# Optimization experiments

Hardware: AMD Instinct MI355X
Metric: run time of the kernel (lower is better)

The kernel has to match this reference:

```python
import jax, jax.numpy as jnp
import numpy as np

PATCH_NUM = 10  # self.patch_num divisor
TOP_N = 5


def _extract_patches(feat, ps):
    """feat: [1,C,H,W] -> [P, C*ps*ps] with P = (H-ps)*(W-ps), matching the
    original loop over h in range(H-ps), w in range(W-ps)."""
    C, H, W = feat.shape[1:]
    Hm, Wm = H - ps, W - ps
    shifts = [feat[0, :, i:i + Hm, j:j + Wm] for i in range(ps) for j in range(ps)]
    patches = jnp.stack(shifts, axis=1)          # [C, ps*ps, Hm, Wm]
    return patches.reshape(C * ps * ps, Hm * Wm).T  # [P, K], P index = h*Wm + w


def _scale_loss(src_f, tgt_f, pos, ps):
    C = src_f.shape[1]
    K = C * ps * ps
    patches = _extract_patches(src_f, ps)  # [P, K]

    def per_target(p):
        th, tw = p[0], p[1]
        tpatch = jax.lax.dynamic_slice(tgt_f, (0, 0, th, tw), (1, C, ps, ps)).reshape(K)
        dist = jnp.sum(jnp.abs(patches - tpatch), axis=1)  # [P] summed L1 per patch
        _, ids = jax.lax.top_k(-dist, TOP_N)                # 5 nearest patches
        sel = patches[ids]                                   # [TOP_N, K]
        # sum over top-n of mean-L1, each divided by top_n (as in original)
        return jnp.sum(jnp.mean(jnp.abs(sel - tpatch), axis=1)) / TOP_N

    # sequential map over the small number of target patches keeps peak memory
    # at one [P,K] abs-diff buffer per step
    return jnp.sum(jax.lax.map(per_target, pos))


def setup_inputs() -> dict:
    key = jax.random.key(0)
    k0, k1, k2, k3, k4, k5 = jax.random.split(key, 6)
    return {
        "src_f0": jax.random.normal(k0, (1, 64, 256, 256), dtype=jnp.float32),
        "tgt_f0": jax.random.normal(k1, (1, 64, 256, 256), dtype=jnp.float32),
        "src_f1": jax.random.normal(k2, (1, 128, 128, 128), dtype=jnp.float32),
        "tgt_f1": jax.random.normal(k3, (1, 128, 128, 128), dtype=jnp.float32),
        "pos0": jax.random.randint(k4, (10, 2), 0, 253, dtype=jnp.int32),
        "pos1": jax.random.randint(k5, (5, 2), 0, 127, dtype=jnp.int32),
    }


def reference(src_f0, tgt_f0, src_f1, tgt_f1, pos0, pos1):
    loss = _scale_loss(src_f0, tgt_f0, pos0, 3) + _scale_loss(src_f1, tgt_f1, pos1, 1)
    return loss / PATCH_NUM
```

## Files before the change

### kernel.cpp

```cpp
#include <hip/hip_runtime.h>
#include <hip/hip_bf16.h>

#define BIG 3.4e38f


__device__ __forceinline__ void merge5(float a[5], const float* b) {
    float r[5];
#pragma unroll
    for (int k = 0; k < 5; ++k) {
        float best = BIG;
#pragma unroll
        for (int i = 0; i <= k + 1; ++i) {
            const int j = k + 1 - i;
            float va = (i == 0) ? -BIG : a[i - 1];
            float vb = (j == 0) ? -BIG : b[j - 1];
            best = fminf(best, fmaxf(va, vb));
        }
        r[k] = best;
    }
#pragma unroll
    for (int k = 0; k < 5; ++k) a[k] = r[k];
}

__device__ __forceinline__ void top5_insert(float m[5], float d) {
    if (d < m[4]) {
        m[4] = d;
#pragma unroll
        for (int k = 4; k > 0; --k) {
            float lo = fminf(m[k - 1], m[k]);
            float hi = fmaxf(m[k - 1], m[k]);
            m[k - 1] = lo;
            m[k] = hi;
        }
    }
}

__device__ __forceinline__ void wave_merge_top5(float m[5]) {
#pragma unroll
    for (int off = 1; off < 64; off <<= 1) {
        float o[5];
#pragma unroll
        for (int k = 0; k < 5; ++k) o[k] = __shfl_xor(m[k], off, 64);
        merge5(m, o);
    }
}

__device__ __forceinline__ bool block_merge_top5(float m[5], float (*s_top)[5],
                                                 float r[5]) {
    const int wid = threadIdx.x >> 6;
    if ((threadIdx.x & 63) == 0) {
#pragma unroll
        for (int k = 0; k < 5; ++k) s_top[wid][k] = m[k];
    }
    __syncthreads();
    if (threadIdx.x == 0) {
#pragma unroll
        for (int k = 0; k < 5; ++k) r[k] = s_top[0][k];
        merge5(r, s_top[1]);
        merge5(r, s_top[2]);
        merge5(r, s_top[3]);
        return true;
    }
    return false;
}

__global__ __launch_bounds__(256) void dist_all_kernel(
    const float* __restrict__ src0, const float* __restrict__ tgt0,
    const int* __restrict__ pos0, const float* __restrict__ src1,
    const float* __restrict__ tgt1, const int* __restrict__ pos1,
    float* __restrict__ dist0, float* __restrict__ p2b) {
    __shared__ float tl[960];
    __shared__ float s_top[4][5];

    if (blockIdx.y < 8) {
        constexpr int H = 256, W = 256, HW = H * W, T = 10, CCH = 8;
        constexpr int PLANE = 253 * 256;
        const int c0 = blockIdx.y * CCH;

        for (int idx = threadIdx.x; idx < T * CCH * 9; idx += 256) {
            int t = idx / (CCH * 9);
            int rem = idx - t * (CCH * 9);
            int cc = rem / 9;
            int r2 = rem - cc * 9;
            int i = r2 / 3, j = r2 - i * 3;
            int th = pos0[2 * t], tw = pos0[2 * t + 1];
            tl[((t * CCH + cc) * 3 + i) * 4 + j] =
                tgt0[(size_t)(c0 + cc) * HW + (th + i) * W + (tw + j)];
        }
        __syncthreads();

        const int tx = threadIdx.x & 63;
        const int ty = threadIdx.x >> 6;
        const int h = blockIdx.x * 4 + ty;
        const int hl = (h <= 250) ? h : 250;
        const int w0 = tx * 4;
        const int bw = (w0 <= 248) ? w0 + 4 : 248;

        float acc[T][4];
#pragma unroll
        for (int t = 0; t < T; ++t)
#pragma unroll
            for (int n = 0; n < 4; ++n) acc[t][n] = 0.f;

        const float* sb = src0 + (size_t)c0 * HW + hl * W;
        for (int cc = 0; cc < CCH; ++cc) {
            const float* row0 = sb + (size_t)cc * HW;
#pragma unroll
            for (int i = 0; i < 3; ++i) {
                const float4 a = *(const float4*)(row0 + i * W + w0);
                const float2 b = *(const float2*)(row0 + i * W + bw);
                const float r[6] = {a.x, a.y, a.z, a.w, b.x, b.y};
#pragma unroll
                for (int t = 0; t < T; ++t) {
                    const float4 tv =
                        *(const float4*)&tl[((t * CCH + cc) * 3 + i) * 4];
#pragma unroll
                    for (int n = 0; n < 4; ++n)
                        acc[t][n] += fabsf(r[n] - tv.x) +
                                     fabsf(r[n + 1] - tv.y) +
                                     fabsf(r[n + 2] - tv.z);
                }
            }
        }

        if (h < 253) {
            float* dp = dist0 + (size_t)blockIdx.y * T * PLANE + h * 256 + w0;
#pragma unroll
            for (int t = 0; t < T; ++t) {
                float4 o = {acc[t][0], acc[t][1], acc[t][2], acc[t][3]};
                *(float4*)(dp + (size_t)t * PLANE) = o;
            }
        }
    } else {
        constexpr int H = 128, W = 128, HW = H * W, T = 5, C = 128;
        for (int idx = threadIdx.x; idx < T * C; idx += 256) {
            int t = idx / C, cc = idx - t * C;
            tl[idx] =
                tgt1[(size_t)cc * HW + pos1[2 * t] * W + pos1[2 * t + 1]];
        }
        __syncthreads();

        const int w = threadIdx.x & 127;
        const int h = blockIdx.x * 2 + (threadIdx.x >> 7);
        float acc[T] = {0.f, 0.f, 0.f, 0.f, 0.f};
        const float* sp = src1 + h * W + w;
        for (int cc = 0; cc < C; ++cc) {
            const float v = sp[(size_t)cc * HW];
#pragma unroll
            for (int t = 0; t < T; ++t) acc[t] += fabsf(v - tl[t * C + cc]);
        }
        const bool valid = (h < 127) && (w < 127);
#pragma unroll
        for (int t = 0; t < T; ++t) {
            float m[5] = {valid ? acc[t] : BIG, BIG, BIG, BIG, BIG};
            wave_merge_top5(m);
            float r[5];
            if (block_merge_top5(m, s_top, r)) {
                float* dst = p2b + (t * 64 + blockIdx.x) * 5;
#pragma unroll
                for (int k = 0; k < 5; ++k) dst[k] = r[k];
            }
            __syncthreads();
        }
    }
}

template <int PLANE, int ROWW, int VALIDW, int NCH, int T, int NB>
__global__ __launch_bounds__(256) void top5_stage_kernel(
    const float* __restrict__ dist, float* __restrict__ part2) {
    __shared__ float s_top[4][5];
    const int t = blockIdx.y;
    constexpr int NF = PLANE / 4;
    constexpr int ITERS = (NF + NB * 256 - 1) / (NB * 256);
    float m[5] = {BIG, BIG, BIG, BIG, BIG};
#pragma unroll
    for (int k = 0; k < ITERS; ++k) {
        const int f = blockIdx.x * (ITERS * 256) + k * 256 + threadIdx.x;
        if (f < NF) {
            float4 s = *(const float4*)&dist[(size_t)t * PLANE + f * 4];
#pragma unroll
            for (int ch = 1; ch < NCH; ++ch) {
                float4 u =
                    *(const float4*)&dist[((size_t)ch * T + t) * PLANE + f * 4];
                s.x += u.x; s.y += u.y; s.z += u.z; s.w += u.w;
            }
            const int w0 = (f * 4) & (ROWW - 1);
            top5_insert(m, (w0 + 0 < VALIDW) ? s.x : BIG);
            top5_insert(m, (w0 + 1 < VALIDW) ? s.y : BIG);
            top5_insert(m, (w0 + 2 < VALIDW) ? s.z : BIG);
            top5_insert(m, (w0 + 3 < VALIDW) ? s.w : BIG);
        }
    }
    wave_merge_top5(m);
    float r[5];
    if (block_merge_top5(m, s_top, r)) {
        float* dst = part2 + (t * NB + blockIdx.x) * 5;
#pragma unroll
        for (int k = 0; k < 5; ++k) dst[k] = r[k];
    }
}

__global__ __launch_bounds__(256) void final_merge_kernel(
    const float* __restrict__ p2a, int na,
    const float* __restrict__ p2b, int nb,
    unsigned int* __restrict__ out) {
    __shared__ float s_sum[15];
    const int lane = threadIdx.x & 63;
    const int wv = threadIdx.x >> 6;
#pragma unroll
    for (int rt = 0; rt < 4; ++rt) {
        const int t = wv * 4 + rt;
        if (t < 15) {
            const float* base = (t < 10) ? p2a + t * na : p2b + (t - 10) * nb;
            const int n = (t < 10) ? na : nb;
            const float scale =
                (t < 10) ? 1.f / (576.f * 5.f) : 1.f / (128.f * 5.f);
            float m[5] = {BIG, BIG, BIG, BIG, BIG};
            for (int b0 = 0; b0 < n; b0 += 64)
                if (b0 + lane < n) top5_insert(m, base[b0 + lane]);
            wave_merge_top5(m);
            if (lane == 0)
                s_sum[t] = (m[0] + m[1] + m[2] + m[3] + m[4]) * scale;
        }
    }
    __syncthreads();
    if (threadIdx.x == 0) {
        float total = 0.f;
#pragma unroll
        for (int t = 0; t < 15; ++t) total += s_sum[t];
        union { float f; unsigned int i; } uf;
        uf.f = total * 0.1f;
        unsigned int bf = (uf.i + 0x7FFFu + ((uf.i >> 16) & 1u)) >> 16;
        out[0] = (uf.i & 0xFFFF0000u) | (bf & 0xFFFFu);
    }
}

template <int C, int H, int PS, int WM>
__global__ __launch_bounds__(256) void dist_top5_kernel(
    const float* __restrict__ src, const float* __restrict__ tgt,
    const int* __restrict__ pos, float* __restrict__ part) {
    constexpr int W = H;
    constexpr int K = C * PS * PS;
    constexpr int P = WM * WM;
    __shared__ float tlv[K];
    __shared__ float s_top[4][5];
    const int t = blockIdx.y;
    const int th = pos[2 * t], tw = pos[2 * t + 1];
    for (int idx = threadIdx.x; idx < K; idx += 256) {
        int c = idx / (PS * PS);
        int rem = idx - c * PS * PS;
        int i = rem / PS, j = rem - i * PS;
        tlv[idx] = tgt[(c * H + th + i) * W + tw + j];
    }
    __syncthreads();
    const int p = blockIdx.x * 256 + threadIdx.x;
    float d = BIG;
    if (p < P) {
        const int h = p / WM, w = p - h * WM;
        float acc = 0.f;
        for (int c = 0; c < C; ++c)
#pragma unroll
            for (int i = 0; i < PS; ++i) {
                const float* r = src + (c * H + h + i) * W + w;
                const float* tr = &tlv[(c * PS + i) * PS];
#pragma unroll
                for (int j = 0; j < PS; ++j) acc += fabsf(r[j] - tr[j]);
            }
        d = acc;
    }
    float m[5] = {d, BIG, BIG, BIG, BIG};
    wave_merge_top5(m);
    float r[5];
    if (block_merge_top5(m, s_top, r)) {
        float* dst = part + (t * gridDim.x + blockIdx.x) * 5;
#pragma unroll
        for (int k = 0; k < 5; ++k) dst[k] = r[k];
    }
}

extern "C" void kernel_launch(void* const* d_in, const int* in_sizes, int n_in,
                              void* d_out, int out_size, void* d_ws, size_t ws_size,
                              hipStream_t stream) {
    const float* src0 = (const float*)d_in[0];
    const float* tgt0 = (const float*)d_in[1];
    const float* src1 = (const float*)d_in[2];
    const float* tgt1 = (const float*)d_in[3];
    const int* pos0 = (const int*)d_in[4];
    const int* pos1 = (const int*)d_in[5];
    unsigned int* out = (unsigned int*)d_out;

    constexpr size_t PLANE0 = 253 * 256;
    constexpr size_t NP2A = 10 * 16 * 5;
    constexpr size_t NP2B = 5 * 64 * 5;
    const size_t need = (8 * 10 * PLANE0 + NP2A + NP2B) * 4;

    if (ws_size >= need) {
        float* dist0 = (float*)d_ws;
        float* p2a = dist0 + 8 * 10 * PLANE0;
        float* p2b = p2a + NP2A;

        dist_all_kernel<<<dim3(64, 9), 256, 0, stream>>>(
            src0, tgt0, pos0, src1, tgt1, pos1, dist0, p2b);
        top5_stage_kernel<253 * 256, 256, 253, 8, 10, 16>
            <<<dim3(16, 10), 256, 0, stream>>>(dist0, p2a);
        final_merge_kernel<<<dim3(1), 256, 0, stream>>>(p2a, 80, p2b, 320, out);
    } else {
        float* part0 = (float*)d_ws;
        float* part1 = part0 + 10 * 251 * 5;
        dist_top5_kernel<64, 256, 3, 253>
            <<<dim3(251, 10), 256, 0, stream>>>(src0, tgt0, pos0, part0);
        dist_top5_kernel<128, 128, 1, 127>
            <<<dim3(64, 5), 256, 0, stream>>>(src1, tgt1, pos1, part1);
        final_merge_kernel<<<dim3(1), 256, 0, stream>>>(part0, 1255, part1, 320, out);
    }
}
```

Measured before the change: 131.1 us.

## Fuse scale-0 distance and top-5 selection, eliminating the dist workspace round-trip

The scale-0 kernel is restructured so each block covers one output row half across all 64 channels, split into four channel groups. The groups are summed through shared memory and a per-block top-5 is taken in the same kernel. This removes the large intermediate distance buffer, its global write and re-read, and the separate top5 stage kernel launch. In exchange it produces many more partial top-5 lists for the final merge, which is widened to load four values per lane per iteration, and it uses much more shared memory per block.

```diff
diff --git a/kernel.cpp b/kernel.cpp
--- a/kernel.cpp
+++ b/kernel.cpp
@@ -68,71 +68,89 @@
     const float* __restrict__ src0, const float* __restrict__ tgt0,
     const int* __restrict__ pos0, const float* __restrict__ src1,
     const float* __restrict__ tgt1, const int* __restrict__ pos1,
-    float* __restrict__ dist0, float* __restrict__ p2b) {
-    __shared__ float tl[960];
+    float* __restrict__ p2a, float* __restrict__ p2b) {
+    __shared__ float tl[10 * 64 * 12];
+    __shared__ float sex[256 * 21];
     __shared__ float s_top[4][5];
 
-    if (blockIdx.y < 8) {
-        constexpr int H = 256, W = 256, HW = H * W, T = 10, CCH = 8;
-        constexpr int PLANE = 253 * 256;
-        const int c0 = blockIdx.y * CCH;
-
-        for (int idx = threadIdx.x; idx < T * CCH * 9; idx += 256) {
-            int t = idx / (CCH * 9);
-            int rem = idx - t * (CCH * 9);
-            int cc = rem / 9;
-            int r2 = rem - cc * 9;
+    const int b = blockIdx.x;
+    if (b < 506) {
+        constexpr int W = 256, HW = 65536, T = 10;
+        const int h = b >> 1;
+        const int wbase = (b & 1) << 7;
+
+        for (int idx = threadIdx.x; idx < T * 64 * 9; idx += 256) {
+            int t = idx / 576;
+            int rem = idx - t * 576;
+            int c = rem / 9;
+            int r2 = rem - c * 9;
             int i = r2 / 3, j = r2 - i * 3;
-            int th = pos0[2 * t], tw = pos0[2 * t + 1];
-            tl[((t * CCH + cc) * 3 + i) * 4 + j] =
-                tgt0[(size_t)(c0 + cc) * HW + (th + i) * W + (tw + j)];
+            tl[((t * 64 + c) * 3 + i) * 4 + j] =
+                tgt0[(size_t)c * HW + (pos0[2 * t] + i) * W +
+                     (pos0[2 * t + 1] + j)];
         }
         __syncthreads();
 
-        const int tx = threadIdx.x & 63;
-        const int ty = threadIdx.x >> 6;
-        const int h = blockIdx.x * 4 + ty;
-        const int hl = (h <= 250) ? h : 250;
-        const int w0 = tx * 4;
-        const int bw = (w0 <= 248) ? w0 + 4 : 248;
-
-        float acc[T][4];
-#pragma unroll
-        for (int t = 0; t < T; ++t)
-#pragma unroll
-            for (int n = 0; n < 4; ++n) acc[t][n] = 0.f;
-
-        const float* sb = src0 + (size_t)c0 * HW + hl * W;
-        for (int cc = 0; cc < CCH; ++cc) {
-            const float* row0 = sb + (size_t)cc * HW;
+        const int p = threadIdx.x & 63;
+        const int q = threadIdx.x >> 6;
+        const int w0 = wbase + 2 * p;
+        const int w0l = (w0 <= 252) ? w0 : 252;
+
+        float acc[T][2];
+#pragma unroll
+        for (int t = 0; t < T; ++t) acc[t][0] = acc[t][1] = 0.f;
+
+        const float* sb = src0 + (size_t)(q * 16) * HW + h * W + w0l;
+        for (int c = 0; c < 16; ++c) {
+            const float* row = sb + (size_t)c * HW;
 #pragma unroll
             for (int i = 0; i < 3; ++i) {
-                const float4 a = *(const float4*)(row0 + i * W + w0);
-                const float2 b = *(const float2*)(row0 + i * W + bw);
-                const float r[6] = {a.x, a.y, a.z, a.w, b.x, b.y};
+                const float4 a = *(const float4*)(row + i * W);
 #pragma unroll
                 for (int t = 0; t < T; ++t) {
-                    const float4 tv =
-                        *(const float4*)&tl[((t * CCH + cc) * 3 + i) * 4];
-#pragma unroll
-                    for (int n = 0; n < 4; ++n)
-                        acc[t][n] += fabsf(r[n] - tv.x) +
-                                     fabsf(r[n + 1] - tv.y) +
-                                     fabsf(r[n + 2] - tv.z);
+                    const float4 tv = *(const float4*)&tl
+                        [((t * 64 + q * 16 + c) * 3 + i) * 4];
+                    acc[t][0] += fabsf(a.x - tv.x) + fabsf(a.y - tv.y) +
+                                 fabsf(a.z - tv.z);
+                    acc[t][1] += fabsf(a.y - tv.x) + fabsf(a.z - tv.y) +
+                                 fabsf(a.w - tv.z);
                 }
             }
         }
 
-        if (h < 253) {
-            float* dp = dist0 + (size_t)blockIdx.y * T * PLANE + h * 256 + w0;
+        {
+            float* se = &sex[threadIdx.x * 21];
 #pragma unroll
             for (int t = 0; t < T; ++t) {
-                float4 o = {acc[t][0], acc[t][1], acc[t][2], acc[t][3]};
-                *(float4*)(dp + (size_t)t * PLANE) = o;
+                se[2 * t] = acc[t][0];
+                se[2 * t + 1] = acc[t][1];
+            }
+        }
+        __syncthreads();
+
+        for (int t = q; t < T; t += 4) {
+            const int ke = 2 * t + (p & 1);
+            const int pr = (p >> 1) * 21;
+            float dlo = 0.f, dhi = 0.f;
+#pragma unroll
+            for (int qq = 0; qq < 4; ++qq) {
+                dlo += sex[qq * 64 * 21 + pr + ke];
+                dhi += sex[qq * 64 * 21 + 32 * 21 + pr + ke];
+            }
+            if (wbase + p >= 253) dlo = BIG;
+            if (wbase + p + 64 >= 253) dhi = BIG;
+            float m[5] = {dlo, BIG, BIG, BIG, BIG};
+            top5_insert(m, dhi);
+            wave_merge_top5(m);
+            if (p == 0) {
+                float* dst = p2a + (t * 506 + b) * 5;
+#pragma unroll
+                for (int k = 0; k < 5; ++k) dst[k] = m[k];
             }
         }
     } else {
-        constexpr int H = 128, W = 128, HW = H * W, T = 5, C = 128;
+        constexpr int W = 128, HW = 16384, T = 5, C = 128;
+        const int bb = b - 506;
         for (int idx = threadIdx.x; idx < T * C; idx += 256) {
             int t = idx / C, cc = idx - t * C;
             tl[idx] =
@@ -141,7 +159,7 @@
         __syncthreads();
 
         const int w = threadIdx.x & 127;
-        const int h = blockIdx.x * 2 + (threadIdx.x >> 7);
+        const int h = bb * 2 + (threadIdx.x >> 7);
         float acc[T] = {0.f, 0.f, 0.f, 0.f, 0.f};
         const float* sp = src1 + h * W + w;
         for (int cc = 0; cc < C; ++cc) {
@@ -156,47 +174,12 @@
             wave_merge_top5(m);
             float r[5];
             if (block_merge_top5(m, s_top, r)) {
-                float* dst = p2b + (t * 64 + blockIdx.x) * 5;
+                float* dst = p2b + (t * 64 + bb) * 5;
 #pragma unroll
                 for (int k = 0; k < 5; ++k) dst[k] = r[k];
             }
             __syncthreads();
         }
-    }
-}
-
-template <int PLANE, int ROWW, int VALIDW, int NCH, int T, int NB>
-__global__ __launch_bounds__(256) void top5_stage_kernel(
-    const float* __restrict__ dist, float* __restrict__ part2) {
-    __shared__ float s_top[4][5];
-    const int t = blockIdx.y;
-    constexpr int NF = PLANE / 4;
-    constexpr int ITERS = (NF + NB * 256 - 1) / (NB * 256);
-    float m[5] = {BIG, BIG, BIG, BIG, BIG};
-#pragma unroll
-    for (int k = 0; k < ITERS; ++k) {
-        const int f = blockIdx.x * (ITERS * 256) + k * 256 + threadIdx.x;
-        if (f < NF) {
-            float4 s = *(const float4*)&dist[(size_t)t * PLANE + f * 4];
-#pragma unroll
-            for (int ch = 1; ch < NCH; ++ch) {
-                float4 u =
-                    *(const float4*)&dist[((size_t)ch * T + t) * PLANE + f * 4];
-                s.x += u.x; s.y += u.y; s.z += u.z; s.w += u.w;
-            }
-            const int w0 = (f * 4) & (ROWW - 1);
-            top5_insert(m, (w0 + 0 < VALIDW) ? s.x : BIG);
-            top5_insert(m, (w0 + 1 < VALIDW) ? s.y : BIG);
-            top5_insert(m, (w0 + 2 < VALIDW) ? s.z : BIG);
-            top5_insert(m, (w0 + 3 < VALIDW) ? s.w : BIG);
-        }
-    }
-    wave_merge_top5(m);
-    float r[5];
-    if (block_merge_top5(m, s_top, r)) {
-        float* dst = part2 + (t * NB + blockIdx.x) * 5;
-#pragma unroll
-        for (int k = 0; k < 5; ++k) dst[k] = r[k];
     }
 }
 
@@ -216,8 +199,16 @@
             const float scale =
                 (t < 10) ? 1.f / (576.f * 5.f) : 1.f / (128.f * 5.f);
             float m[5] = {BIG, BIG, BIG, BIG, BIG};
-            for (int b0 = 0; b0 < n; b0 += 64)
-                if (b0 + lane < n) top5_insert(m, base[b0 + lane]);
+            for (int b0 = 0; b0 < n; b0 += 256) {
+                float v[4];
+#pragma unroll
+                for (int j = 0; j < 4; ++j) {
+                    const int idx = b0 + j * 64 + lane;
+                    v[j] = (idx < n) ? base[idx] : BIG;
+                }
+#pragma unroll
+                for (int j = 0; j < 4; ++j) top5_insert(m, v[j]);
+            }
             wave_merge_top5(m);
             if (lane == 0)
                 s_sum[t] = (m[0] + m[1] + m[2] + m[3] + m[4]) * scale;
@@ -289,21 +280,18 @@
     const int* pos1 = (const int*)d_in[5];
     unsigned int* out = (unsigned int*)d_out;
 
-    constexpr size_t PLANE0 = 253 * 256;
-    constexpr size_t NP2A = 10 * 16 * 5;
+    constexpr size_t NP2A = 10 * 506 * 5;
     constexpr size_t NP2B = 5 * 64 * 5;
-    const size_t need = (8 * 10 * PLANE0 + NP2A + NP2B) * 4;
+    const size_t need = (NP2A + NP2B) * 4;
 
     if (ws_size >= need) {
-        float* dist0 = (float*)d_ws;
-        float* p2a = dist0 + 8 * 10 * PLANE0;
+        float* p2a = (float*)d_ws;
         float* p2b = p2a + NP2A;
 
-        dist_all_kernel<<<dim3(64, 9), 256, 0, stream>>>(
-            src0, tgt0, pos0, src1, tgt1, pos1, dist0, p2b);
-        top5_stage_kernel<253 * 256, 256, 253, 8, 10, 16>
-            <<<dim3(16, 10), 256, 0, stream>>>(dist0, p2a);
-        final_merge_kernel<<<dim3(1), 256, 0, stream>>>(p2a, 80, p2b, 320, out);
+        dist_all_kernel<<<dim3(570), 256, 0, stream>>>(
+            src0, tgt0, pos0, src1, tgt1, pos1, p2a, p2b);
+        final_merge_kernel<<<dim3(1), 256, 0, stream>>>(
+            p2a, 506 * 5, p2b, 320, out);
     } else {
         float* part0 = (float*)d_ws;
         float* part1 = part0 + 10 * 251 * 5;
```

Result: slower. 154.3 us (+17.6%).
